# Optimization experiments

Measured on AMD Instinct MI355X. Metric: run time of the kernel, lower is better.

## Reference

```python
import jax, jax.numpy as jnp
import numpy as np

B, S, D_MODEL, H = 2, 2048, 1024, 16
DK = D_MODEL // H
THETA = 10000.0


def setup_inputs() -> dict:
    key = jax.random.key(0)
    ks = jax.random.split(key, 5)
    scale = 0.02  # keep logits in a numerically sane range
    return {
        "x": jax.random.normal(ks[0], (B, S, D_MODEL), jnp.float32),
        "Q_weight": jax.random.normal(ks[1], (D_MODEL, D_MODEL), jnp.float32) * scale,
        "K_weight": jax.random.normal(ks[2], (D_MODEL, D_MODEL), jnp.float32) * scale,
        "V_weight": jax.random.normal(ks[3], (D_MODEL, D_MODEL), jnp.float32) * scale,
        "O_weight": jax.random.normal(ks[4], (D_MODEL, D_MODEL), jnp.float32) * scale,
        "token_positions": jnp.arange(S, dtype=jnp.int32),
    }


def _rope(x, token_positions, theta, d_k):
    # x: [..., seq, d_k]; rotate interleaved even/odd pairs
    inv_freq = 1.0 / theta ** (jnp.arange(0, d_k, 2, dtype=jnp.float32) / d_k)
    ang = token_positions.astype(jnp.float32)[:, None] * inv_freq  # [S, d_k/2]
    cos, sin = jnp.cos(ang), jnp.sin(ang)
    x0, x1 = x[..., 0::2], x[..., 1::2]
    y0 = x0 * cos - x1 * sin
    y1 = x0 * sin + x1 * cos
    return jnp.stack([y0, y1], axis=-1).reshape(x.shape)


def _mhsa(x, Qw, Kw, Vw, Ow, token_positions):
    b, s, d = x.shape
    qw = Qw.reshape(H, DK, d)
    kw = Kw.reshape(H, DK, d)
    vw = Vw.reshape(H, DK, d)
    q = jnp.einsum('hki,bsi->bhsk', qw, x)
    k = jnp.einsum('hki,bsi->bhsk', kw, x)
    v = jnp.einsum('hvi,bsi->bhsv', vw, x)
    q = _rope(q, token_positions, THETA, DK)
    k = _rope(k, token_positions, THETA, DK)
    scores = jnp.einsum('bhnd,bhmd->bhnm', q, k) / jnp.sqrt(jnp.float32(DK))
    causal = jnp.tril(jnp.ones((s, s), dtype=bool))
    scores = jnp.where(causal, scores, -jnp.inf)
    attn = jax.nn.softmax(scores, axis=-1)
    o = jnp.einsum('bhnm,bhmv->bhnv', attn, v)  # [B,H,S,DV]
    o = jnp.transpose(o, (0, 2, 1, 3)).reshape(b, s, H * DK)
    return jnp.einsum('dv,bsv->bsd', Ow, o)


def reference(x, Q_weight, K_weight, V_weight, O_weight, token_positions):
    return _mhsa(x, Q_weight, K_weight, V_weight, O_weight, token_positions)
```

## Files before the change

kernel.cpp:

```cpp
#include <hip/hip_runtime.h>

#define NB 2
#define NS 2048
#define NDM 1024
#define NH 16
#define NDK 64

typedef unsigned int u32;
typedef u32 u32x4 __attribute__((ext_vector_type(4)));
typedef float f32x4 __attribute__((ext_vector_type(4)));
typedef float f32x2 __attribute__((ext_vector_type(2)));
typedef __bf16 bf16x8 __attribute__((ext_vector_type(8)));
typedef __bf16 bf16x4 __attribute__((ext_vector_type(4)));
typedef __bf16 bf16x2 __attribute__((ext_vector_type(2)));

#define QSCALE 0.18033688011112042f
#define EXP2F(x) __builtin_amdgcn_exp2f(x)

__device__ __forceinline__ void gload_lds16(const __bf16* g, __bf16* l) {
    __builtin_amdgcn_global_load_lds(
        (const __attribute__((address_space(1))) unsigned int*)(g),
        (__attribute__((address_space(3))) unsigned int*)(l), 16, 0, 0);
}

__global__ __launch_bounds__(256) void cvt_all(const float* __restrict__ x,
                                               const float* __restrict__ qw,
                                               const float* __restrict__ kw,
                                               const float* __restrict__ vw,
                                               const float* __restrict__ ow,
                                               __bf16* __restrict__ xb,
                                               __bf16* __restrict__ wqkv,
                                               __bf16* __restrict__ owb) {
    const int i = blockIdx.x * 256 + threadIdx.x;
    const float* src;
    __bf16* dst;
    if (i < 1048576) {
        src = x + (size_t)i * 4;
        dst = xb + (size_t)i * 4;
    } else {
        const int j = i - 1048576;
        const int seg = j >> 18;
        const int off = j & 0x3FFFF;
        src = ((seg == 0) ? qw : (seg == 1) ? kw : (seg == 2) ? vw : ow) + (size_t)off * 4;
        dst = ((seg == 3) ? owb : wqkv + (size_t)seg * 1048576) + (size_t)off * 4;
    }
    f32x4 v = *(const f32x4*)src;
    bf16x4 o;
    o[0] = (__bf16)v[0]; o[1] = (__bf16)v[1]; o[2] = (__bf16)v[2]; o[3] = (__bf16)v[3];
    *(bf16x4*)dst = o;
}

__global__ __launch_bounds__(256) void rope_table(const int* __restrict__ tp,
                                                  float* __restrict__ tbl) {
    const int i = blockIdx.x * 256 + threadIdx.x;
    if (i >= NS * 32) return;
    const int s = i >> 5, jj = i & 31;
    const float pos = (float)tp[s];
    const float inv = exp2f(-0.41524101186092f * (float)jj);
    const float ang = pos * inv;
    float sn, cs;
    sincosf(ang, &sn, &cs);
    f32x2 o; o[0] = cs; o[1] = sn;
    *(f32x2*)&tbl[(size_t)i * 2] = o;
}

__global__ __launch_bounds__(512, 2) void gemm256(const __bf16* __restrict__ A,
                                                  const __bf16* __restrict__ Bt,
                                                  __bf16* __restrict__ C,
                                                  int K, int lda, int ldb, int ldc, int nbx) {
    __shared__ __bf16 As[2][256 * 64];
    __shared__ __bf16 Bs[2][256 * 64];
    const int tid = threadIdx.x;
    const int lane = tid & 63, w = tid >> 6;
    const int wm = w >> 2, wn = w & 3;
    const int l15 = lane & 15, lg = lane >> 4;
    int bid = blockIdx.x;
    const int cpx = gridDim.x >> 3;
    bid = (bid & 7) * cpx + (bid >> 3);
    const int m0 = (bid / nbx) * 256, n0 = (bid % nbx) * 256;
    const int srow = w * 8 + (lane >> 3);
    const int csw = ((lane & 7) ^ (srow & 7)) * 8;

    f32x4 acc[8][4];
    const f32x4 z = {0.f, 0.f, 0.f, 0.f};
#pragma unroll
    for (int i = 0; i < 8; ++i)
#pragma unroll
        for (int jx = 0; jx < 4; ++jx) acc[i][jx] = z;

    auto stage = [&](int buf, int k0) {
#pragma unroll
        for (int ps = 0; ps < 4; ++ps) {
            const int r = ps * 64 + srow;
            gload_lds16(&A[(size_t)(m0 + r) * lda + k0 + csw], &As[buf][(ps * 64 + w * 8) * 64]);
        }
#pragma unroll
        for (int ps = 0; ps < 4; ++ps) {
            const int r = ps * 64 + srow;
            gload_lds16(&Bt[(size_t)(n0 + r) * ldb + k0 + csw], &Bs[buf][(ps * 64 + w * 8) * 64]);
        }
    };

    stage(0, 0);
    int cur = 0;
    for (int k0 = 0; k0 < K; k0 += 64) {
        if (k0 + 64 < K) {
            stage(cur ^ 1, k0 + 64);
            asm volatile("s_waitcnt vmcnt(8)" ::: "memory");
        } else {
            asm volatile("s_waitcnt vmcnt(0)" ::: "memory");
        }
        __builtin_amdgcn_s_barrier();
        __builtin_amdgcn_sched_barrier(0);
        bf16x8 bfr[4][2];
#pragma unroll
        for (int n = 0; n < 4; ++n)
#pragma unroll
            for (int kc = 0; kc < 2; ++kc) {
                const int rb = wn * 64 + n * 16 + l15;
                bfr[n][kc] = *(const bf16x8*)&Bs[cur][rb * 64 + ((kc * 32 + lg * 8) ^ ((rb & 7) << 3))];
            }
#pragma unroll
        for (int mr = 0; mr < 8; ++mr) {
            bf16x8 af[2];
#pragma unroll
            for (int kc = 0; kc < 2; ++kc) {
                const int ra = wm * 128 + mr * 16 + l15;
                af[kc] = *(const bf16x8*)&As[cur][ra * 64 + ((kc * 32 + lg * 8) ^ ((ra & 7) << 3))];
            }
#pragma unroll
            for (int n = 0; n < 4; ++n)
#pragma unroll
                for (int kc = 0; kc < 2; ++kc)
                    acc[mr][n] = __builtin_amdgcn_mfma_f32_16x16x32_bf16(af[kc], bfr[n][kc], acc[mr][n], 0, 0, 0);
        }
        asm volatile("s_waitcnt lgkmcnt(0)" ::: "memory");
        __builtin_amdgcn_s_barrier();
        __builtin_amdgcn_sched_barrier(0);
        cur ^= 1;
    }
#pragma unroll
    for (int mr = 0; mr < 8; ++mr)
#pragma unroll
        for (int n = 0; n < 4; ++n)
#pragma unroll
            for (int j = 0; j < 4; ++j) {
                const int row = m0 + wm * 128 + mr * 16 + lg * 4 + j;
                const int col = n0 + wn * 64 + n * 16 + l15;
                C[(size_t)row * ldc + col] = (__bf16)acc[mr][n][j];
            }
}

template <typename TOUT>
__global__ __launch_bounds__(256) void gemm_bt128(const __bf16* __restrict__ A,
                                                  const __bf16* __restrict__ Bt,
                                                  TOUT* __restrict__ C,
                                                  int K, int lda, int ldb, int ldc) {
    __shared__ __bf16 As[2][128 * 64];
    __shared__ __bf16 Bs[2][128 * 64];
    const int tid = threadIdx.x;
    const int lane = tid & 63, w = tid >> 6;
    const int wr = w >> 1, wc = w & 1;
    const int l15 = lane & 15, lg = lane >> 4;
    const int m0 = blockIdx.y * 128, n0 = blockIdx.x * 128;
    const int crow = lane >> 3;
    const int csw = ((lane & 7) ^ crow) * 8;

    f32x4 acc[4][4];
    const f32x4 z = {0.f, 0.f, 0.f, 0.f};
#pragma unroll
    for (int i = 0; i < 4; ++i)
#pragma unroll
        for (int jx = 0; jx < 4; ++jx) acc[i][jx] = z;

    auto stage = [&](int buf, int k0) {
#pragma unroll
        for (int ch = 0; ch < 4; ++ch) {
            const int cid = w * 4 + ch;
            const int ra = cid * 8 + crow;
            gload_lds16(&A[(size_t)(m0 + ra) * lda + k0 + csw], &As[buf][cid * 512]);
            gload_lds16(&Bt[(size_t)(n0 + ra) * ldb + k0 + csw], &Bs[buf][cid * 512]);
        }
    };

    stage(0, 0);
    int cur = 0;
    for (int k0 = 0; k0 < K; k0 += 64) {
        if (k0 + 64 < K) {
            stage(cur ^ 1, k0 + 64);
            asm volatile("s_waitcnt vmcnt(8)" ::: "memory");
        } else {
            asm volatile("s_waitcnt vmcnt(0)" ::: "memory");
        }
        __builtin_amdgcn_s_barrier();
        __builtin_amdgcn_sched_barrier(0);
#pragma unroll
        for (int kc = 0; kc < 2; ++kc) {
            bf16x8 af[4], bfv[4];
#pragma unroll
            for (int i = 0; i < 4; ++i) {
                const int ra = wr * 64 + i * 16 + l15;
                const int rb = wc * 64 + i * 16 + l15;
                af[i]  = *(const bf16x8*)&As[cur][ra * 64 + ((kc * 32 + lg * 8) ^ ((ra & 7) << 3))];
                bfv[i] = *(const bf16x8*)&Bs[cur][rb * 64 + ((kc * 32 + lg * 8) ^ ((rb & 7) << 3))];
            }
#pragma unroll
            for (int sm = 0; sm < 4; ++sm)
#pragma unroll
                for (int sn = 0; sn < 4; ++sn)
                    acc[sm][sn] = __builtin_amdgcn_mfma_f32_16x16x32_bf16(af[sm], bfv[sn], acc[sm][sn], 0, 0, 0);
        }
        asm volatile("s_waitcnt lgkmcnt(0)" ::: "memory");
        __builtin_amdgcn_s_barrier();
        __builtin_amdgcn_sched_barrier(0);
        cur ^= 1;
    }
#pragma unroll
    for (int sm = 0; sm < 4; ++sm)
#pragma unroll
        for (int sn = 0; sn < 4; ++sn)
#pragma unroll
            for (int j = 0; j < 4; ++j) {
                const int row = m0 + wr * 64 + sm * 16 + lg * 4 + j;
                const int col = n0 + wc * 64 + sn * 16 + l15;
                C[(size_t)row * ldc + col] = (TOUT)acc[sm][sn][j];
            }
}

__global__ __launch_bounds__(512) void rope_kernel(const __bf16* __restrict__ qkv,
                                                   const float* __restrict__ tbl,
                                                   __bf16* __restrict__ Qr,
                                                   __bf16* __restrict__ Kr) {
    const int row = blockIdx.x;
    const int s = row & (NS - 1);
    const int b = row >> 11;
    const int t = threadIdx.x;
    const int h = t >> 5, jj = t & 31;
    f32x2 cssn = *(const f32x2*)&tbl[((size_t)s * 32 + jj) * 2];
    const float cs = cssn[0], sn = cssn[1];
    const __bf16* qp = qkv + (size_t)row * 3072 + h * 64 + 2 * jj;
    bf16x2 qv = *(const bf16x2*)qp;
    bf16x2 kv = *(const bf16x2*)(qp + 1024);
    const float q0 = (float)qv[0], q1 = (float)qv[1];
    const float k0 = (float)kv[0], k1 = (float)kv[1];
    const size_t o = ((size_t)(b * NH + h) * NS + s) * 64 + 2 * jj;
    bf16x2 qo, ko;
    qo[0] = (__bf16)((q0 * cs - q1 * sn) * QSCALE);
    qo[1] = (__bf16)((q0 * sn + q1 * cs) * QSCALE);
    ko[0] = (__bf16)(k0 * cs - k1 * sn); ko[1] = (__bf16)(k0 * sn + k1 * cs);
    *(bf16x2*)&Qr[o] = qo;
    *(bf16x2*)&Kr[o] = ko;
}

__global__ __launch_bounds__(256) void vtrans(const __bf16* __restrict__ qkv,
                                              __bf16* __restrict__ Vt) {
    const int bh = blockIdx.y;
    const int s0 = blockIdx.x * 64;
    const int b = bh >> 4, h = bh & 15;
    __shared__ __bf16 tile[64][72];
    const int t = threadIdx.x;
    const int sl = t >> 3, c8 = (t & 7) * 8;
#pragma unroll
    for (int pp = 0; pp < 2; ++pp) {
        const int srow = sl + pp * 32;
        bf16x8 v = *(const bf16x8*)&qkv[(size_t)(b * NS + s0 + srow) * 3072 + 2048 + h * 64 + c8];
        *(bf16x8*)&tile[srow][c8] = v;
    }
    __syncthreads();
    const int d = t >> 2;
#pragma unroll
    for (int pp = 0; pp < 2; ++pp) {
        const int vec = (t & 3) + pp * 4;
        bf16x8 o;
#pragma unroll
        for (int i = 0; i < 8; ++i) o[i] = tile[vec * 8 + i][d];
        *(bf16x8*)&Vt[((size_t)bh * 64 + d) * NS + s0 + vec * 8] = o;
    }
}

__device__ __forceinline__ int kperm(int rt) {
    const int ct = rt >> 4, rr = rt & 15;
    return ((rr >> 2) << 3) + ((ct >> 1) << 5) + ((ct & 1) << 2) + (rr & 3);
}

__global__ __launch_bounds__(256) void attn5(const __bf16* __restrict__ Qr,
                                             const __bf16* __restrict__ Kr,
                                             const __bf16* __restrict__ Vt,
                                             __bf16* __restrict__ O) {
    const int lid = blockIdx.x;
    const int xcd = lid & 7, ix = lid >> 3;
    const int bh = xcd * 4 + (ix & 3);
    const int p  = ix >> 2;
    const int b = bh >> 4, h = bh & 15;
    const int tid = threadIdx.x;
    const int w = tid >> 6, lane = tid & 63;
    const int l15 = lane & 15, lg = lane >> 4;
    const __bf16* Qb = Qr + (size_t)bh * NS * 64;
    const __bf16* Kb = Kr + (size_t)bh * NS * 64;
    const __bf16* Vb = Vt + (size_t)bh * 64 * NS;

    __shared__ __bf16 Ks[2][64 * 64];
    __shared__ __bf16 Vs[2][64 * 64];

    const int rbv[2] = {p * 64 + w * 16, (31 - p) * 64 + w * 16};

    bf16x8 qf[2][2];
#pragma unroll
    for (int rs = 0; rs < 2; ++rs)
#pragma unroll
        for (int kc = 0; kc < 2; ++kc)
            qf[rs][kc] = *(const bf16x8*)(Qb + (size_t)(rbv[rs] + l15) * 64 + kc * 32 + lg * 8);

    f32x4 oacc[2][4];
    const f32x4 z = {0.f, 0.f, 0.f, 0.f};
#pragma unroll
    for (int rs = 0; rs < 2; ++rs)
#pragma unroll
        for (int ct = 0; ct < 4; ++ct) oacc[rs][ct] = z;
    float lsum[2] = {0.f, 0.f};

    const int crow = lane >> 3;
    const int cswz = ((lane & 7) ^ crow) * 8;

#pragma unroll
    for (int pp = 0; pp < 2; ++pp) {
        const int ch = w + pp * 4;
        const int rt = ch * 8 + crow;
        gload_lds16(Kb + (size_t)kperm(rt) * 64 + cswz, &Ks[0][ch * 512]);
        gload_lds16(Vb + (size_t)rt * NS + 0 + cswz, &Vs[0][ch * 512]);
    }
    __syncthreads();

    const int nt = 32 - p;
    for (int t = 0; t < nt; ++t) {
        const int cur = t & 1;
        const int kv0 = t << 6;
        if (t + 1 < nt) {
            const int kv1 = kv0 + 64;
#pragma unroll
            for (int pp = 0; pp < 2; ++pp) {
                const int ch = w + pp * 4;
                const int rt = ch * 8 + crow;
                gload_lds16(Kb + (size_t)(kv1 + kperm(rt)) * 64 + cswz, &Ks[cur ^ 1][ch * 512]);
                gload_lds16(Vb + (size_t)rt * NS + kv1 + cswz, &Vs[cur ^ 1][ch * 512]);
            }
        }
        bool act[2];
        act[0] = (kv0 <= rbv[0] + 15);
        act[1] = true;
        f32x4 sc[2][4];
#pragma unroll
        for (int rs = 0; rs < 2; ++rs)
            if (act[rs])
#pragma unroll
                for (int ct = 0; ct < 4; ++ct) sc[rs][ct] = z;
#pragma unroll
        for (int kc = 0; kc < 2; ++kc) {
            bf16x8 kf[4];
#pragma unroll
            for (int ct = 0; ct < 4; ++ct) {
                const int rt = ct * 16 + l15;
                kf[ct] = *(const bf16x8*)&Ks[cur][rt * 64 + ((kc * 32 + lg * 8) ^ ((rt & 7) << 3))];
            }
#pragma unroll
            for (int rs = 0; rs < 2; ++rs)
                if (act[rs])
#pragma unroll
                    for (int ct = 0; ct < 4; ++ct)
                        sc[rs][ct] = __builtin_amdgcn_mfma_f32_16x16x32_bf16(kf[ct], qf[rs][kc], sc[rs][ct], 0, 0, 0);
        }
        bf16x8 pb[2][2];
#pragma unroll
        for (int rs = 0; rs < 2; ++rs) {
            if (!act[rs]) continue;
            const int rbase = rbv[rs];
            const int qrow = rbase + l15;
            const bool needmask = (kv0 + 63 > rbase);
            if (needmask) {
#pragma unroll
                for (int ct = 0; ct < 4; ++ct)
#pragma unroll
                    for (int j = 0; j < 4; ++j) {
                        const int kvg = kv0 + ((ct >> 1) << 5) + lg * 8 + ((ct & 1) << 2) + j;
                        if (kvg > qrow) sc[rs][ct][j] = -1e30f;
                    }
            }
            float ps = 0.f;
#pragma unroll
            for (int ct = 0; ct < 4; ++ct)
#pragma unroll
                for (int j = 0; j < 4; ++j) {
                    const float e = EXP2F(sc[rs][ct][j]);
                    sc[rs][ct][j] = e;
                    ps += e;
                }
            ps += __shfl_xor(ps, 16, 64);
            ps += __shfl_xor(ps, 32, 64);
            lsum[rs] += ps;
#pragma unroll
            for (int kc = 0; kc < 2; ++kc) {
                bf16x8 pk;
                pk[0] = (__bf16)sc[rs][2 * kc][0];     pk[1] = (__bf16)sc[rs][2 * kc][1];
                pk[2] = (__bf16)sc[rs][2 * kc][2];     pk[3] = (__bf16)sc[rs][2 * kc][3];
                pk[4] = (__bf16)sc[rs][2 * kc + 1][0]; pk[5] = (__bf16)sc[rs][2 * kc + 1][1];
                pk[6] = (__bf16)sc[rs][2 * kc + 1][2]; pk[7] = (__bf16)sc[rs][2 * kc + 1][3];
                pb[rs][kc] = pk;
            }
        }
#pragma unroll
        for (int kc = 0; kc < 2; ++kc) {
            bf16x8 vf[4];
#pragma unroll
            for (int ct = 0; ct < 4; ++ct) {
                const int rt = ct * 16 + l15;
                vf[ct] = *(const bf16x8*)&Vs[cur][rt * 64 + ((kc * 32 + lg * 8) ^ ((rt & 7) << 3))];
            }
#pragma unroll
            for (int rs = 0; rs < 2; ++rs) {
                if (!act[rs]) continue;
#pragma unroll
                for (int ct = 0; ct < 4; ++ct)
                    oacc[rs][ct] = __builtin_amdgcn_mfma_f32_16x16x32_bf16(vf[ct], pb[rs][kc], oacc[rs][ct], 0, 0, 0);
            }
        }
        __syncthreads();
    }
#pragma unroll
    for (int rs = 0; rs < 2; ++rs) {
        const float rl = 1.0f / lsum[rs];
        const size_t rowoff = (size_t)(b * NS + rbv[rs] + l15) * NDM + h * 64 + lg * 4;
#pragma unroll
        for (int ct = 0; ct < 4; ++ct) {
            bf16x4 ov;
#pragma unroll
            for (int j = 0; j < 4; ++j) ov[j] = (__bf16)(oacc[rs][ct][j] * rl);
            *(bf16x4*)&O[rowoff + ct * 16] = ov;
        }
    }
}

extern "C" void kernel_launch(void* const* d_in, const int* in_sizes, int n_in,
                              void* d_out, int out_size, void* d_ws, size_t ws_size,
                              hipStream_t stream) {
    const float* x  = (const float*)d_in[0];
    const float* Qw = (const float*)d_in[1];
    const float* Kw = (const float*)d_in[2];
    const float* Vw = (const float*)d_in[3];
    const float* Ow = (const float*)d_in[4];
    const int*   tp = (const int*)d_in[5];
    float* out = (float*)d_out;

    char* ws = (char*)d_ws;
    size_t off = 0;
    auto alloc = [&](size_t bytes) -> void* {
        void* p = ws + off;
        off += (bytes + 255) & ~(size_t)255;
        return p;
    };
    __bf16* xb   = (__bf16*)alloc((size_t)4096 * 1024 * 2);
    __bf16* wqkv = (__bf16*)alloc((size_t)3072 * 1024 * 2);
    __bf16* owb  = (__bf16*)alloc((size_t)1024 * 1024 * 2);
    __bf16* qkv  = (__bf16*)alloc((size_t)4096 * 3072 * 2);
    __bf16* qr   = (__bf16*)alloc((size_t)32 * 2048 * 64 * 2);
    __bf16* kr   = (__bf16*)alloc((size_t)32 * 2048 * 64 * 2);
    __bf16* vt   = (__bf16*)alloc((size_t)32 * 64 * 2048 * 2);
    __bf16* ob   = (__bf16*)alloc((size_t)4096 * 1024 * 2);
    float*  tbl  = (float*)alloc((size_t)NS * 32 * 2 * 4);

    cvt_all<<<8192, 256, 0, stream>>>(x, Qw, Kw, Vw, Ow, xb, wqkv, owb);
    rope_table<<<(NS * 32 + 255) / 256, 256, 0, stream>>>(tp, tbl);

    gemm256<<<192, 512, 0, stream>>>(xb, wqkv, qkv, 1024, 1024, 1024, 3072, 12);
    rope_kernel<<<4096, 512, 0, stream>>>(qkv, tbl, qr, kr);
    vtrans<<<dim3(NS / 64, NB * NH), 256, 0, stream>>>(qkv, vt);
    attn5<<<dim3(512), 256, 0, stream>>>(qr, kr, vt, ob);
    gemm_bt128<float><<<dim3(1024 / 128, 4096 / 128), 256, 0, stream>>>(
        ob, owb, out, 1024, 1024, 1024, 1024);
}
```

Measured before the change: 118.8 us.

## Interleave next-tile staging with MFMA phases in 256x256 GEMM main loop

```diff
diff --git a/kernel.cpp b/kernel.cpp
--- a/kernel.cpp
+++ b/kernel.cpp
@@ -88,55 +88,56 @@
 #pragma unroll
         for (int jx = 0; jx < 4; ++jx) acc[i][jx] = z;
 
-    auto stage = [&](int buf, int k0) {
-#pragma unroll
-        for (int ps = 0; ps < 4; ++ps) {
-            const int r = ps * 64 + srow;
-            gload_lds16(&A[(size_t)(m0 + r) * lda + k0 + csw], &As[buf][(ps * 64 + w * 8) * 64]);
-        }
-#pragma unroll
-        for (int ps = 0; ps < 4; ++ps) {
-            const int r = ps * 64 + srow;
-            gload_lds16(&Bt[(size_t)(n0 + r) * ldb + k0 + csw], &Bs[buf][(ps * 64 + w * 8) * 64]);
-        }
+    auto stage_pass = [&](int buf, int k0, int ps) {
+        const int r = ps * 64 + srow;
+        gload_lds16(&A[(size_t)(m0 + r) * lda + k0 + csw], &As[buf][(ps * 64 + w * 8) * 64]);
+        gload_lds16(&Bt[(size_t)(n0 + r) * ldb + k0 + csw], &Bs[buf][(ps * 64 + w * 8) * 64]);
     };
 
-    stage(0, 0);
+#pragma unroll
+    for (int ps = 0; ps < 4; ++ps) stage_pass(0, 0, ps);
     int cur = 0;
     for (int k0 = 0; k0 < K; k0 += 64) {
-        if (k0 + 64 < K) {
-            stage(cur ^ 1, k0 + 64);
-            asm volatile("s_waitcnt vmcnt(8)" ::: "memory");
-        } else {
-            asm volatile("s_waitcnt vmcnt(0)" ::: "memory");
-        }
+        const bool hasnext = (k0 + 64 < K);
+        asm volatile("s_waitcnt vmcnt(0)" ::: "memory");
         __builtin_amdgcn_s_barrier();
         __builtin_amdgcn_sched_barrier(0);
         bf16x8 bfr[4][2];
 #pragma unroll
-        for (int n = 0; n < 4; ++n)
+        for (int ph = 0; ph < 4; ++ph) {
+            if (ph == 0) {
+#pragma unroll
+                for (int n = 0; n < 4; ++n)
+#pragma unroll
+                    for (int kc = 0; kc < 2; ++kc) {
+                        const int rb = wn * 64 + n * 16 + l15;
+                        bfr[n][kc] = *(const bf16x8*)&Bs[cur][rb * 64 + ((kc * 32 + lg * 8) ^ ((rb & 7) << 3))];
+                    }
+            }
+            bf16x8 a0[2], a1[2];
 #pragma unroll
             for (int kc = 0; kc < 2; ++kc) {
-                const int rb = wn * 64 + n * 16 + l15;
-                bfr[n][kc] = *(const bf16x8*)&Bs[cur][rb * 64 + ((kc * 32 + lg * 8) ^ ((rb & 7) << 3))];
-            }
-#pragma unroll
-        for (int mr = 0; mr < 8; ++mr) {
-            bf16x8 af[2];
-#pragma unroll
-            for (int kc = 0; kc < 2; ++kc) {
-                const int ra = wm * 128 + mr * 16 + l15;
-                af[kc] = *(const bf16x8*)&As[cur][ra * 64 + ((kc * 32 + lg * 8) ^ ((ra & 7) << 3))];
-            }
+                const int ra0 = wm * 128 + (2 * ph) * 16 + l15;
+                const int ra1 = wm * 128 + (2 * ph + 1) * 16 + l15;
+                a0[kc] = *(const bf16x8*)&As[cur][ra0 * 64 + ((kc * 32 + lg * 8) ^ ((ra0 & 7) << 3))];
+                a1[kc] = *(const bf16x8*)&As[cur][ra1 * 64 + ((kc * 32 + lg * 8) ^ ((ra1 & 7) << 3))];
+            }
+            if (hasnext) stage_pass(cur ^ 1, k0 + 64, ph);
+            __builtin_amdgcn_s_barrier();
+            asm volatile("s_waitcnt lgkmcnt(0)" ::: "memory");
+            __builtin_amdgcn_sched_barrier(0);
+            __builtin_amdgcn_s_setprio(1);
 #pragma unroll
             for (int n = 0; n < 4; ++n)
 #pragma unroll
-                for (int kc = 0; kc < 2; ++kc)
-                    acc[mr][n] = __builtin_amdgcn_mfma_f32_16x16x32_bf16(af[kc], bfr[n][kc], acc[mr][n], 0, 0, 0);
-        }
-        asm volatile("s_waitcnt lgkmcnt(0)" ::: "memory");
-        __builtin_amdgcn_s_barrier();
-        __builtin_amdgcn_sched_barrier(0);
+                for (int kc = 0; kc < 2; ++kc) {
+                    acc[2 * ph][n]     = __builtin_amdgcn_mfma_f32_16x16x32_bf16(a0[kc], bfr[n][kc], acc[2 * ph][n], 0, 0, 0);
+                    acc[2 * ph + 1][n] = __builtin_amdgcn_mfma_f32_16x16x32_bf16(a1[kc], bfr[n][kc], acc[2 * ph + 1][n], 0, 0, 0);
+                }
+            __builtin_amdgcn_s_setprio(0);
+            __builtin_amdgcn_s_barrier();
+            __builtin_amdgcn_sched_barrier(0);
+        }
         cur ^= 1;
     }
 #pragma unroll
```

Measured after the change: 119.8 us. About the same (+0.9%).
